# Performance work log

Hardware: AMD Instinct MI355X
Metric: run time of the kernel (lower is better)

Reference implementation:

```python
import jax, jax.numpy as jnp
import numpy as np

NB, NA, NC, NH, NW = 64, 5, 20, 38, 38
MAXT = 40
ANCHORS = jnp.array([[1.3221, 1.73145], [3.19275, 4.00944], [5.05587, 8.09892],
                     [9.47112, 4.84053], [11.2364, 10.0071]], dtype=jnp.float32)
OBJECT_SCALE, NOOBJECT_SCALE = 5.0, 1.0
CLASS_SCALE, COORD_SCALE = 1.0, 1.0
THRESH = 0.4


def setup_inputs() -> dict:
    key = jax.random.key(0)
    k1, k2, k3, k4 = jax.random.split(key, 4)
    output = jax.random.normal(k1, (NB, NA * (5 + NC), NH, NW), dtype=jnp.float32)
    cls_id = jax.random.randint(k2, (NB, MAXT), 0, NC).astype(jnp.float32)
    gxy = jax.random.uniform(k3, (NB, MAXT, 2), minval=0.05, maxval=0.95)
    gwh = jax.random.uniform(k4, (NB, MAXT, 2), minval=0.05, maxval=0.5)
    target = jnp.concatenate([cls_id[..., None], gxy, gwh], axis=-1).reshape(NB, MAXT * 5)
    return {"output": output, "target": target}


def iou_cwh(a, b):
    # boxes in (cx, cy, w, h)
    ax1, ax2 = a[..., 0] - a[..., 2] * 0.5, a[..., 0] + a[..., 2] * 0.5
    ay1, ay2 = a[..., 1] - a[..., 3] * 0.5, a[..., 1] + a[..., 3] * 0.5
    bx1, bx2 = b[..., 0] - b[..., 2] * 0.5, b[..., 0] + b[..., 2] * 0.5
    by1, by2 = b[..., 1] - b[..., 3] * 0.5, b[..., 1] + b[..., 3] * 0.5
    iw = jnp.maximum(jnp.minimum(ax2, bx2) - jnp.maximum(ax1, bx1), 0.0)
    ih = jnp.maximum(jnp.minimum(ay2, by2) - jnp.maximum(ay1, by1), 0.0)
    inter = iw * ih
    union = a[..., 2] * a[..., 3] + b[..., 2] * b[..., 3] - inter
    return inter / union


def smooth_l1_sum(p, t):
    d = jnp.abs(p - t)
    return jnp.sum(jnp.where(d < 1.0, 0.5 * d * d, d - 0.5))


def _forward(output, target):
    nB, nA, nC, nH, nW = NB, NA, NC, NH, NW
    out5 = output.reshape(nB, nA, 5 + nC, nH, nW)
    x = jax.nn.sigmoid(out5[:, :, 0])      # [nB,nA,nH,nW]
    y = jax.nn.sigmoid(out5[:, :, 1])
    w = out5[:, :, 2]
    h = out5[:, :, 3]
    conf = jax.nn.sigmoid(out5[:, :, 4])
    cls_logits = jnp.transpose(out5[:, :, 5:], (0, 1, 3, 4, 2))  # [nB,nA,nH,nW,nC]

    # --- decode predicted boxes (detached, mirrors use of .data in torch) ---
    sg = jax.lax.stop_gradient
    grid_x = jnp.arange(nW, dtype=jnp.float32)[None, None, None, :]
    grid_y = jnp.arange(nH, dtype=jnp.float32)[None, None, :, None]
    aw = ANCHORS[:, 0][None, :, None, None]
    ah = ANCHORS[:, 1][None, :, None, None]
    pred = jnp.stack([sg(x) + grid_x, sg(y) + grid_y,
                      jnp.exp(sg(w)) * aw, jnp.exp(sg(h)) * ah], axis=-1)  # [nB,nA,nH,nW,4]

    # --- build_targets (vectorized) ---
    tgt = target.reshape(nB, MAXT, 5)
    gcls = tgt[..., 0]
    gx, gy = tgt[..., 1] * nW, tgt[..., 2] * nH
    gw, gh = tgt[..., 3] * nW, tgt[..., 4] * nH
    # loop breaks at first zero gx: all later targets invalid
    valid = jnp.cumprod((tgt[..., 1] != 0).astype(jnp.float32), axis=1) > 0  # [nB,40]

    gt_boxes = jnp.stack([gx, gy, gw, gh], axis=-1)                 # [nB,40,4]
    pb = pred.reshape(nB, nA * nH * nW, 4)
    ious = iou_cwh(gt_boxes[:, :, None, :], pb[:, None, :, :])      # [nB,40,nAnchors]
    ious = jnp.where(valid[:, :, None], ious, 0.0)
    cur_ious = jnp.max(ious, axis=1)                                # [nB,nAnchors]
    conf_mask = jnp.where(cur_ious > THRESH, 0.0, NOOBJECT_SCALE).reshape(nB, nA, nH, nW)

    # best anchor per GT: IoU of zero-centered (w,h) boxes
    aws, ahs = ANCHORS[:, 0], ANCHORS[:, 1]
    inter = jnp.minimum(gw[..., None], aws) * jnp.minimum(gh[..., None], ahs)
    a_iou = inter / (gw[..., None] * gh[..., None] + aws * ahs - inter)  # [nB,40,nA]
    best_n = jnp.argmax(a_iou, axis=-1)                                  # [nB,40]

    gi = jnp.clip(gx.astype(jnp.int32), 0, nW - 1)
    gj = jnp.clip(gy.astype(jnp.int32), 0, nH - 1)
    bidx = jnp.broadcast_to(jnp.arange(nB)[:, None], (nB, MAXT))
    gi_s = jnp.where(valid, gi, nW)  # out-of-bounds -> dropped scatter
    idx = (bidx, best_n, gj, gi_s)

    pred_sel = pred[bidx, best_n, gj, gi]        # [nB,40,4]
    t_iou = iou_cwh(gt_boxes, pred_sel)          # [nB,40]
    aw_b, ah_b = aws[best_n], ahs[best_n]
    vtx = gx - gi.astype(jnp.float32)
    vty = gy - gj.astype(jnp.float32)
    vtw = jnp.log(gw / aw_b)
    vth = jnp.log(gh / ah_b)

    zeros = jnp.zeros((nB, nA, nH, nW), dtype=jnp.float32)
    coord_mask = zeros.at[idx].set(1.0, mode='drop')
    cls_mask = coord_mask  # identical writes in torch code
    conf_mask = conf_mask.at[idx].set(OBJECT_SCALE, mode='drop')
    tx = zeros.at[idx].set(vtx, mode='drop')
    ty = zeros.at[idx].set(vty, mode='drop')
    tw = zeros.at[idx].set(vtw, mode='drop')
    th = zeros.at[idx].set(vth, mode='drop')
    tconf = zeros.at[idx].set(t_iou, mode='drop')
    tcls = jnp.zeros((nB, nA, nH, nW), dtype=jnp.int32).at[idx].set(gcls.astype(jnp.int32), mode='drop')

    coord_mask = sg(coord_mask); cls_mask = sg(cls_mask)
    conf_mask = sg(conf_mask)
    tx, ty, tw, th, tconf = sg(tx), sg(ty), sg(tw), sg(th), sg(tconf)

    # --- losses ---
    loss_x = COORD_SCALE * smooth_l1_sum(x * coord_mask, tx * coord_mask) / 2.0
    loss_y = COORD_SCALE * smooth_l1_sum(y * coord_mask, ty * coord_mask) / 2.0
    loss_w = COORD_SCALE * smooth_l1_sum(w * coord_mask, tw * coord_mask) / 2.0
    loss_h = COORD_SCALE * smooth_l1_sum(h * coord_mask, th * coord_mask) / 2.0
    cm = jnp.sqrt(conf_mask)
    loss_conf = jnp.sum((conf * cm - tconf * cm) ** 2) / 2.0
    # focal loss (gamma=2, sum) over cls-masked locations
    logp = jax.nn.log_softmax(cls_logits, axis=-1)
    logpt = jnp.take_along_axis(logp, tcls[..., None], axis=-1)[..., 0]
    pt = jnp.exp(logpt)
    fl = -((1.0 - pt) ** 2) * logpt
    loss_cls = CLASS_SCALE * jnp.sum(cls_mask * fl)

    loss_box = loss_x + loss_y + loss_w + loss_h + loss_conf
    loss = loss_box + loss_cls
    return loss, loss_cls, loss_box


def reference(output, target):
    return _forward(output, target)
```

## Files before the change

### kernel.cpp

```cpp
#include <hip/hip_runtime.h>

#define NB 64
#define NA 5
#define NC 20
#define NH 38
#define NW 38
#define MAXT 40
#define CS (NH * NW)
#define CELLS_PER_B (NA * CS)
#define TPB 256
#define CPT 2
#define CHUNK_CELLS (TPB * CPT)
#define CHUNKS 16
#define NBLK (NB * CHUNKS)
#define IOUC (0.4f / 1.4f)

__constant__ float c_aw[NA] = {1.3221f, 3.19275f, 5.05587f, 9.47112f, 11.2364f};
__constant__ float c_ah[NA] = {1.73145f, 4.00944f, 8.09892f, 4.84053f, 10.0071f};

__device__ __forceinline__ float sl1(float d) {
    d = fabsf(d);
    return (d < 1.0f) ? 0.5f * d * d : d - 0.5f;
}
__device__ __forceinline__ float sigm(float x) {
    return __builtin_amdgcn_rcpf(1.0f + __expf(-x));
}

__global__ __launch_bounds__(TPB) void region_kernel(
    const float* __restrict__ outp, const float* __restrict__ tgt,
    float2* __restrict__ partials)
{
    __shared__ float4 s_box[MAXT];
    __shared__ alignas(16) float s_ga[MAXT];
    __shared__ int    s_key[MAXT];

    const int b     = blockIdx.x >> 4;
    const int chunk = blockIdx.x & 15;
    const int tid   = threadIdx.x;

    const int cbase = chunk * CHUNK_CELLS + tid;
    float xo[CPT], yo[CPT], wo[CPT], ho[CPT], co[CPT];
    bool live[CPT];
    #pragma unroll
    for (int u = 0; u < CPT; ++u) {
        const int c  = cbase + u * TPB;
        live[u] = (c < CELLS_PER_B);
        const int cc = live[u] ? c : (CELLS_PER_B - 1);
        const int a  = cc / CS, r = cc - a * CS;
        const float* cell = outp + (size_t)((b * NA + a) * (5 + NC)) * CS + r;
        xo[u] = cell[0];      yo[u] = cell[CS];
        wo[u] = cell[2 * CS]; ho[u] = cell[3 * CS];
        co[u] = cell[4 * CS];
    }

    float w_gx = 0.f, w_gy = 0.f, w_gw = 0.f, w_gh = 0.f;
    int   w_bn = 0, w_gi = 0, w_gj = 0, w_cls = 0, mykey = -1;
    bool  w_valid = false;

    if (tid < 64) {
        const bool is_t = tid < MAXT;
        const float* tb = tgt + b * (MAXT * 5) + tid * 5;
        float t0 = 0.f, t1 = 0.f, t2 = 0.f, t3 = 0.f, t4 = 0.f;
        if (is_t) { t0 = tb[0]; t1 = tb[1]; t2 = tb[2]; t3 = tb[3]; t4 = tb[4]; }
        const unsigned long long nz = __ballot(is_t && (t1 != 0.0f));
        const bool valid = is_t && ((~nz & (((1ull << tid) << 1) - 1ull)) == 0ull);
        if (is_t) {
            float4 mybox = make_float4(3e30f, 3e30f, -3e30f, -3e30f);
            float  myga  = 0.0f;
            if (valid) {
                const float gx = t1 * NW, gy = t2 * NH, gw = t3 * NW, gh = t4 * NH;
                int bn = 0; float best = -1.0f;
                #pragma unroll
                for (int a = 0; a < NA; ++a) {
                    const float inter = fminf(gw, c_aw[a]) * fminf(gh, c_ah[a]);
                    const float aiou  = inter / (gw * gh + c_aw[a] * c_ah[a] - inter);
                    if (aiou > best) { best = aiou; bn = a; }
                }
                const int gi = min(max((int)gx, 0), NW - 1);
                const int gj = min(max((int)gy, 0), NH - 1);
                mybox = make_float4(gx - 0.5f * gw, gy - 0.5f * gh,
                                    gx + 0.5f * gw, gy + 0.5f * gh);
                myga  = IOUC * (gw * gh);
                mykey = bn * CS + gj * NW + gi;
                w_gx = gx; w_gy = gy; w_gw = gw; w_gh = gh;
                w_bn = bn; w_gi = gi; w_gj = gj; w_cls = (int)t0; w_valid = true;
            }
            s_box[tid] = mybox; s_ga[tid] = myga; s_key[tid] = valid ? mykey : -1;
        }
    }

    float px1[CPT], px2[CPT], py1[CPT], py2[CPT], p04[CPT], scv[CPT];
    #pragma unroll
    for (int u = 0; u < CPT; ++u) {
        const int c = cbase + u * TPB;
        const int cc = live[u] ? c : 0;
        const int a = cc / CS, r = cc - a * CS;
        const int j = r / NW,  i = r - j * NW;
        const float sx = sigm(xo[u]), sy = sigm(yo[u]);
        scv[u] = live[u] ? sigm(co[u]) : 0.0f;
        const float pxc = sx + (float)i, pyc = sy + (float)j;
        const float pw = __expf(wo[u]) * c_aw[a], ph = __expf(ho[u]) * c_ah[a];
        px1[u] = pxc - 0.5f * pw; px2[u] = pxc + 0.5f * pw;
        py1[u] = pyc - 0.5f * ph; py2[u] = pyc + 0.5f * ph;
        p04[u] = IOUC * (pw * ph);
    }

    __syncthreads();

    float box_sum = 0.0f, cls_sum = 0.0f;

    if (chunk == CHUNKS - 1 && w_valid) {
        bool last = true;
        for (int tp = tid + 1; tp < MAXT; ++tp) last &= (s_key[tp] != mykey);
        if (last) {
            const float* cell = outp + (size_t)((b * NA + w_bn) * (5 + NC)) * CS
                                + (w_gj * NW + w_gi);
            const float xw = cell[0],      yw = cell[CS];
            const float ww = cell[2 * CS], hw = cell[3 * CS], cw = cell[4 * CS];
            float cls_v[NC];
            #pragma unroll
            for (int q = 0; q < NC; ++q) cls_v[q] = cell[(5 + q) * CS];

            const float sx = sigm(xw), sy = sigm(yw), sc = sigm(cw);
            const float pxc = sx + (float)w_gi, pyc = sy + (float)w_gj;
            const float pw = __expf(ww) * c_aw[w_bn], ph = __expf(hw) * c_ah[w_bn];
            const float wx1 = pxc - 0.5f * pw, wx2 = pxc + 0.5f * pw;
            const float wy1 = pyc - 0.5f * ph, wy2 = pyc + 0.5f * ph;
            const float pa = pw * ph, wp04 = IOUC * (pw * ph);

            bool flag = false;
            for (int t = 0; t < MAXT; ++t) {
                const float4 bx = s_box[t];
                const float iw = fminf(wx2, bx.z) - fmaxf(wx1, bx.x);
                const float ih = fminf(wy2, bx.w) - fmaxf(wy1, bx.y);
                const float inter = fmaxf(iw, 0.0f) * fmaxf(ih, 0.0f);
                flag = flag | (inter > wp04 + s_ga[t]);
            }
            const float cmd = flag ? 0.0f : 1.0f;

            const float gx1 = w_gx - 0.5f * w_gw, gx2 = w_gx + 0.5f * w_gw;
            const float gy1 = w_gy - 0.5f * w_gh, gy2 = w_gy + 0.5f * w_gh;
            const float iw = fminf(wx2, gx2) - fmaxf(wx1, gx1);
            const float ih = fminf(wy2, gy2) - fmaxf(wy1, gy1);
            const float inter = fmaxf(iw, 0.f) * fmaxf(ih, 0.f);
            const float tconf = inter / (w_gw * w_gh + pa - inter);

            const float dc = sc - tconf;
            box_sum += 2.5f * dc * dc - 0.5f * cmd * sc * sc;

            const float vtx = w_gx - (float)w_gi, vty = w_gy - (float)w_gj;
            const float vtw = __logf(w_gw / c_aw[w_bn]);
            const float vth = __logf(w_gh / c_ah[w_bn]);
            box_sum += 0.5f * (sl1(sx - vtx) + sl1(sy - vty) +
                               sl1(ww - vtw) + sl1(hw - vth));

            float m = -1e30f;
            #pragma unroll
            for (int q = 0; q < NC; ++q) m = fmaxf(m, cls_v[q]);
            float se = 0.f, lt = 0.f;
            #pragma unroll
            for (int q = 0; q < NC; ++q) {
                se += __expf(cls_v[q] - m);
                if (q == w_cls) lt = cls_v[q];
            }
            const float logpt = lt - (m + __logf(se));
            const float pt = __expf(logpt);
            const float om = 1.0f - pt;
            cls_sum += -(om * om) * logpt;
        }
    } else if (chunk != CHUNKS - 1) {
        bool flag[CPT];
        #pragma unroll
        for (int u = 0; u < CPT; ++u) flag[u] = false;

        #pragma unroll 2
        for (int t4 = 0; t4 < MAXT; t4 += 4) {
            const float4 ga4 = *reinterpret_cast<const float4*>(&s_ga[t4]);
            #pragma unroll
            for (int k = 0; k < 4; ++k) {
                const float4 bx = s_box[t4 + k];
                const float  ga = (k == 0) ? ga4.x : (k == 1) ? ga4.y
                                 : (k == 2) ? ga4.z : ga4.w;
                #pragma unroll
                for (int u = 0; u < CPT; ++u) {
                    const float iw = fminf(px2[u], bx.z) - fmaxf(px1[u], bx.x);
                    const float ih = fminf(py2[u], bx.w) - fmaxf(py1[u], bx.y);
                    const float inter = fmaxf(iw, 0.0f) * fmaxf(ih, 0.0f);
                    flag[u] = flag[u] | (inter > p04[u] + ga);
                }
            }
        }

        #pragma unroll
        for (int u = 0; u < CPT; ++u) {
            if (!flag[u]) box_sum += 0.5f * scv[u] * scv[u];
        }
    }

    #pragma unroll
    for (int off = 32; off > 0; off >>= 1) {
        box_sum += __shfl_down(box_sum, off);
        cls_sum += __shfl_down(cls_sum, off);
    }
    __shared__ float red[8];
    const int wv = tid >> 6, ln = tid & 63;
    if (ln == 0) { red[wv] = box_sum; red[4 + wv] = cls_sum; }
    __syncthreads();
    if (tid == 0) {
        partials[blockIdx.x] = make_float2(red[0] + red[1] + red[2] + red[3],
                                           red[4] + red[5] + red[6] + red[7]);
    }
}

__global__ __launch_bounds__(256) void finalize_kernel(
    const float2* __restrict__ partials, float* __restrict__ o)
{
    const int tid = threadIdx.x;
    float box = 0.0f, cls = 0.0f;
    #pragma unroll
    for (int k = 0; k < 4; ++k) {
        const float2 p = partials[tid + k * 256];
        box += p.x; cls += p.y;
    }
    #pragma unroll
    for (int off = 32; off > 0; off >>= 1) {
        box += __shfl_down(box, off);
        cls += __shfl_down(cls, off);
    }
    __shared__ float red[8];
    const int wv = tid >> 6, ln = tid & 63;
    if (ln == 0) { red[wv] = box; red[4 + wv] = cls; }
    __syncthreads();
    if (tid == 0) {
        const float boxT = red[0] + red[1] + red[2] + red[3];
        const float clsT = red[4] + red[5] + red[6] + red[7];
        o[0] = boxT + clsT;
        o[1] = clsT;
        o[2] = boxT;
    }
}

extern "C" void kernel_launch(void* const* d_in, const int* in_sizes, int n_in,
                              void* d_out, int out_size, void* d_ws, size_t ws_size,
                              hipStream_t stream)
{
    const float* outp = (const float*)d_in[0];
    const float* tgt  = (const float*)d_in[1];
    float2* partials  = (float2*)d_ws;

    region_kernel<<<dim3(NBLK), dim3(TPB), 0, stream>>>(outp, tgt, partials);
    finalize_kernel<<<1, 256, 0, stream>>>(partials, (float*)d_out);
}
```

Baseline: 18.05 us.

## Broadcast target boxes via readlane per wave, split last-chunk path from LDS

The non-last chunks now compute the target boxes redundantly in every wave and broadcast them with readlane, with no shared-memory staging. This removes the block-wide barrier and the LDS reads from the main IoU loop, which is now fully unrolled. The last chunk keeps the shared-memory path and its own barrier. In exchange, every wave repeats the target loads and box math, and the unrolled loop adds 200 readlane instructions.

```diff
diff --git a/kernel.cpp b/kernel.cpp
--- a/kernel.cpp
+++ b/kernel.cpp
@@ -25,169 +25,189 @@
 __device__ __forceinline__ float sigm(float x) {
     return __builtin_amdgcn_rcpf(1.0f + __expf(-x));
 }
+__device__ __forceinline__ float rdlane(float v, int l) {
+    return __int_as_float(__builtin_amdgcn_readlane(__float_as_int(v), l));
+}
 
 __global__ __launch_bounds__(TPB) void region_kernel(
     const float* __restrict__ outp, const float* __restrict__ tgt,
     float2* __restrict__ partials)
 {
     __shared__ float4 s_box[MAXT];
-    __shared__ alignas(16) float s_ga[MAXT];
+    __shared__ float  s_ga[MAXT];
     __shared__ int    s_key[MAXT];
+    __shared__ float  red[8];
 
     const int b     = blockIdx.x >> 4;
     const int chunk = blockIdx.x & 15;
     const int tid   = threadIdx.x;
-
-    const int cbase = chunk * CHUNK_CELLS + tid;
-    float xo[CPT], yo[CPT], wo[CPT], ho[CPT], co[CPT];
-    bool live[CPT];
-    #pragma unroll
-    for (int u = 0; u < CPT; ++u) {
-        const int c  = cbase + u * TPB;
-        live[u] = (c < CELLS_PER_B);
-        const int cc = live[u] ? c : (CELLS_PER_B - 1);
-        const int a  = cc / CS, r = cc - a * CS;
-        const float* cell = outp + (size_t)((b * NA + a) * (5 + NC)) * CS + r;
-        xo[u] = cell[0];      yo[u] = cell[CS];
-        wo[u] = cell[2 * CS]; ho[u] = cell[3 * CS];
-        co[u] = cell[4 * CS];
-    }
-
-    float w_gx = 0.f, w_gy = 0.f, w_gw = 0.f, w_gh = 0.f;
-    int   w_bn = 0, w_gi = 0, w_gj = 0, w_cls = 0, mykey = -1;
-    bool  w_valid = false;
-
-    if (tid < 64) {
-        const bool is_t = tid < MAXT;
-        const float* tb = tgt + b * (MAXT * 5) + tid * 5;
-        float t0 = 0.f, t1 = 0.f, t2 = 0.f, t3 = 0.f, t4 = 0.f;
-        if (is_t) { t0 = tb[0]; t1 = tb[1]; t2 = tb[2]; t3 = tb[3]; t4 = tb[4]; }
-        const unsigned long long nz = __ballot(is_t && (t1 != 0.0f));
-        const bool valid = is_t && ((~nz & (((1ull << tid) << 1) - 1ull)) == 0ull);
-        if (is_t) {
-            float4 mybox = make_float4(3e30f, 3e30f, -3e30f, -3e30f);
-            float  myga  = 0.0f;
+    const int lane  = tid & 63;
+
+    float box_sum = 0.0f, cls_sum = 0.0f;
+
+    if (chunk == CHUNKS - 1) {
+        float w_gx = 0.f, w_gy = 0.f, w_gw = 0.f, w_gh = 0.f;
+        int   w_bn = 0, w_gi = 0, w_gj = 0, w_cls = 0, mykey = -1;
+        bool  w_valid = false;
+
+        if (tid < 64) {
+            const bool is_t = tid < MAXT;
+            const float* tb = tgt + b * (MAXT * 5) + tid * 5;
+            float t0 = 0.f, t1 = 0.f, t2 = 0.f, t3 = 0.f, t4 = 0.f;
+            if (is_t) { t0 = tb[0]; t1 = tb[1]; t2 = tb[2]; t3 = tb[3]; t4 = tb[4]; }
+            const unsigned long long nz = __ballot(is_t && (t1 != 0.0f));
+            const bool valid = is_t && ((~nz & (((1ull << tid) << 1) - 1ull)) == 0ull);
+            if (is_t) {
+                float4 mybox = make_float4(3e30f, 3e30f, -3e30f, -3e30f);
+                float  myga  = 0.0f;
+                if (valid) {
+                    const float gx = t1 * NW, gy = t2 * NH, gw = t3 * NW, gh = t4 * NH;
+                    int bn = 0; float best = -1.0f;
+                    #pragma unroll
+                    for (int a = 0; a < NA; ++a) {
+                        const float inter = fminf(gw, c_aw[a]) * fminf(gh, c_ah[a]);
+                        const float aiou  = inter / (gw * gh + c_aw[a] * c_ah[a] - inter);
+                        if (aiou > best) { best = aiou; bn = a; }
+                    }
+                    const int gi = min(max((int)gx, 0), NW - 1);
+                    const int gj = min(max((int)gy, 0), NH - 1);
+                    mybox = make_float4(gx - 0.5f * gw, gy - 0.5f * gh,
+                                        gx + 0.5f * gw, gy + 0.5f * gh);
+                    myga  = IOUC * (gw * gh);
+                    mykey = bn * CS + gj * NW + gi;
+                    w_gx = gx; w_gy = gy; w_gw = gw; w_gh = gh;
+                    w_bn = bn; w_gi = gi; w_gj = gj; w_cls = (int)t0; w_valid = true;
+                }
+                s_box[tid] = mybox; s_ga[tid] = myga; s_key[tid] = valid ? mykey : -1;
+            }
+        }
+        __syncthreads();
+
+        if (w_valid) {
+            bool last = true;
+            for (int tp = tid + 1; tp < MAXT; ++tp) last &= (s_key[tp] != mykey);
+            if (last) {
+                const float* cell = outp + (size_t)((b * NA + w_bn) * (5 + NC)) * CS
+                                    + (w_gj * NW + w_gi);
+                const float xw = cell[0],      yw = cell[CS];
+                const float ww = cell[2 * CS], hw = cell[3 * CS], cw = cell[4 * CS];
+                float cls_v[NC];
+                #pragma unroll
+                for (int q = 0; q < NC; ++q) cls_v[q] = cell[(5 + q) * CS];
+
+                const float sx = sigm(xw), sy = sigm(yw), sc = sigm(cw);
+                const float pxc = sx + (float)w_gi, pyc = sy + (float)w_gj;
+                const float pw = __expf(ww) * c_aw[w_bn], ph = __expf(hw) * c_ah[w_bn];
+                const float wx1 = pxc - 0.5f * pw, wx2 = pxc + 0.5f * pw;
+                const float wy1 = pyc - 0.5f * ph, wy2 = pyc + 0.5f * ph;
+                const float pa = pw * ph, wp04 = IOUC * (pw * ph);
+
+                bool flag = false;
+                for (int t = 0; t < MAXT; ++t) {
+                    const float4 bx = s_box[t];
+                    const float iw = fminf(wx2, bx.z) - fmaxf(wx1, bx.x);
+                    const float ih = fminf(wy2, bx.w) - fmaxf(wy1, bx.y);
+                    const float inter = fmaxf(iw, 0.0f) * fmaxf(ih, 0.0f);
+                    flag = flag | (inter > wp04 + s_ga[t]);
+                }
+                const float cmd = flag ? 0.0f : 1.0f;
+
+                const float gx1 = w_gx - 0.5f * w_gw, gx2 = w_gx + 0.5f * w_gw;
+                const float gy1 = w_gy - 0.5f * w_gh, gy2 = w_gy + 0.5f * w_gh;
+                const float iw = fminf(wx2, gx2) - fmaxf(wx1, gx1);
+                const float ih = fminf(wy2, gy2) - fmaxf(wy1, gy1);
+                const float inter = fmaxf(iw, 0.f) * fmaxf(ih, 0.f);
+                const float tconf = inter / (w_gw * w_gh + pa - inter);
+
+                const float dc = sc - tconf;
+                box_sum += 2.5f * dc * dc - 0.5f * cmd * sc * sc;
+
+                const float vtx = w_gx - (float)w_gi, vty = w_gy - (float)w_gj;
+                const float vtw = __logf(w_gw / c_aw[w_bn]);
+                const float vth = __logf(w_gh / c_ah[w_bn]);
+                box_sum += 0.5f * (sl1(sx - vtx) + sl1(sy - vty) +
+                                   sl1(ww - vtw) + sl1(hw - vth));
+
+                float m = -1e30f;
+                #pragma unroll
+                for (int q = 0; q < NC; ++q) m = fmaxf(m, cls_v[q]);
+                float se = 0.f, lt = 0.f;
+                #pragma unroll
+                for (int q = 0; q < NC; ++q) {
+                    se += __expf(cls_v[q] - m);
+                    if (q == w_cls) lt = cls_v[q];
+                }
+                const float logpt = lt - (m + __logf(se));
+                const float pt = __expf(logpt);
+                const float om = 1.0f - pt;
+                cls_sum += -(om * om) * logpt;
+            }
+        }
+    } else {
+        const int cbase = chunk * CHUNK_CELLS + tid;
+        float xo[CPT], yo[CPT], wo[CPT], ho[CPT], co[CPT];
+        bool live[CPT];
+        #pragma unroll
+        for (int u = 0; u < CPT; ++u) {
+            const int c  = cbase + u * TPB;
+            live[u] = (c < CELLS_PER_B);
+            const int cc = live[u] ? c : (CELLS_PER_B - 1);
+            const int a  = cc / CS, r = cc - a * CS;
+            const float* cell = outp + (size_t)((b * NA + a) * (5 + NC)) * CS + r;
+            xo[u] = cell[0];      yo[u] = cell[CS];
+            wo[u] = cell[2 * CS]; ho[u] = cell[3 * CS];
+            co[u] = cell[4 * CS];
+        }
+
+        float x1v = 3e30f, y1v = 3e30f, x2v = -3e30f, y2v = -3e30f, gav = 0.0f;
+        {
+            const bool is_t = lane < MAXT;
+            const float* tb = tgt + b * (MAXT * 5) + lane * 5;
+            float t1 = 0.f, t2 = 0.f, t3 = 0.f, t4 = 0.f;
+            if (is_t) { t1 = tb[1]; t2 = tb[2]; t3 = tb[3]; t4 = tb[4]; }
+            const unsigned long long nz = __ballot(is_t && (t1 != 0.0f));
+            const bool valid = is_t && ((~nz & (((1ull << lane) << 1) - 1ull)) == 0ull);
             if (valid) {
                 const float gx = t1 * NW, gy = t2 * NH, gw = t3 * NW, gh = t4 * NH;
-                int bn = 0; float best = -1.0f;
-                #pragma unroll
-                for (int a = 0; a < NA; ++a) {
-                    const float inter = fminf(gw, c_aw[a]) * fminf(gh, c_ah[a]);
-                    const float aiou  = inter / (gw * gh + c_aw[a] * c_ah[a] - inter);
-                    if (aiou > best) { best = aiou; bn = a; }
-                }
-                const int gi = min(max((int)gx, 0), NW - 1);
-                const int gj = min(max((int)gy, 0), NH - 1);
-                mybox = make_float4(gx - 0.5f * gw, gy - 0.5f * gh,
-                                    gx + 0.5f * gw, gy + 0.5f * gh);
-                myga  = IOUC * (gw * gh);
-                mykey = bn * CS + gj * NW + gi;
-                w_gx = gx; w_gy = gy; w_gw = gw; w_gh = gh;
-                w_bn = bn; w_gi = gi; w_gj = gj; w_cls = (int)t0; w_valid = true;
-            }
-            s_box[tid] = mybox; s_ga[tid] = myga; s_key[tid] = valid ? mykey : -1;
-        }
-    }
-
-    float px1[CPT], px2[CPT], py1[CPT], py2[CPT], p04[CPT], scv[CPT];
-    #pragma unroll
-    for (int u = 0; u < CPT; ++u) {
-        const int c = cbase + u * TPB;
-        const int cc = live[u] ? c : 0;
-        const int a = cc / CS, r = cc - a * CS;
-        const int j = r / NW,  i = r - j * NW;
-        const float sx = sigm(xo[u]), sy = sigm(yo[u]);
-        scv[u] = live[u] ? sigm(co[u]) : 0.0f;
-        const float pxc = sx + (float)i, pyc = sy + (float)j;
-        const float pw = __expf(wo[u]) * c_aw[a], ph = __expf(ho[u]) * c_ah[a];
-        px1[u] = pxc - 0.5f * pw; px2[u] = pxc + 0.5f * pw;
-        py1[u] = pyc - 0.5f * ph; py2[u] = pyc + 0.5f * ph;
-        p04[u] = IOUC * (pw * ph);
-    }
-
-    __syncthreads();
-
-    float box_sum = 0.0f, cls_sum = 0.0f;
-
-    if (chunk == CHUNKS - 1 && w_valid) {
-        bool last = true;
-        for (int tp = tid + 1; tp < MAXT; ++tp) last &= (s_key[tp] != mykey);
-        if (last) {
-            const float* cell = outp + (size_t)((b * NA + w_bn) * (5 + NC)) * CS
-                                + (w_gj * NW + w_gi);
-            const float xw = cell[0],      yw = cell[CS];
-            const float ww = cell[2 * CS], hw = cell[3 * CS], cw = cell[4 * CS];
-            float cls_v[NC];
+                x1v = gx - 0.5f * gw; y1v = gy - 0.5f * gh;
+                x2v = gx + 0.5f * gw; y2v = gy + 0.5f * gh;
+                gav = IOUC * (gw * gh);
+            }
+        }
+
+        float px1[CPT], px2[CPT], py1[CPT], py2[CPT], p04[CPT], scv[CPT];
+        #pragma unroll
+        for (int u = 0; u < CPT; ++u) {
+            const int c = cbase + u * TPB;
+            const int cc = live[u] ? c : 0;
+            const int a = cc / CS, r = cc - a * CS;
+            const int j = r / NW,  i = r - j * NW;
+            const float sx = sigm(xo[u]), sy = sigm(yo[u]);
+            scv[u] = live[u] ? sigm(co[u]) : 0.0f;
+            const float pxc = sx + (float)i, pyc = sy + (float)j;
+            const float pw = __expf(wo[u]) * c_aw[a], ph = __expf(ho[u]) * c_ah[a];
+            px1[u] = pxc - 0.5f * pw; px2[u] = pxc + 0.5f * pw;
+            py1[u] = pyc - 0.5f * ph; py2[u] = pyc + 0.5f * ph;
+            p04[u] = IOUC * (pw * ph);
+        }
+
+        bool flag[CPT];
+        #pragma unroll
+        for (int u = 0; u < CPT; ++u) flag[u] = false;
+
+        #pragma unroll
+        for (int t = 0; t < MAXT; ++t) {
+            const float bx1 = rdlane(x1v, t);
+            const float by1 = rdlane(y1v, t);
+            const float bx2 = rdlane(x2v, t);
+            const float by2 = rdlane(y2v, t);
+            const float ga  = rdlane(gav, t);
             #pragma unroll
-            for (int q = 0; q < NC; ++q) cls_v[q] = cell[(5 + q) * CS];
-
-            const float sx = sigm(xw), sy = sigm(yw), sc = sigm(cw);
-            const float pxc = sx + (float)w_gi, pyc = sy + (float)w_gj;
-            const float pw = __expf(ww) * c_aw[w_bn], ph = __expf(hw) * c_ah[w_bn];
-            const float wx1 = pxc - 0.5f * pw, wx2 = pxc + 0.5f * pw;
-            const float wy1 = pyc - 0.5f * ph, wy2 = pyc + 0.5f * ph;
-            const float pa = pw * ph, wp04 = IOUC * (pw * ph);
-
-            bool flag = false;
-            for (int t = 0; t < MAXT; ++t) {
-                const float4 bx = s_box[t];
-                const float iw = fminf(wx2, bx.z) - fmaxf(wx1, bx.x);
-                const float ih = fminf(wy2, bx.w) - fmaxf(wy1, bx.y);
+            for (int u = 0; u < CPT; ++u) {
+                const float iw = fminf(px2[u], bx2) - fmaxf(px1[u], bx1);
+                const float ih = fminf(py2[u], by2) - fmaxf(py1[u], by1);
                 const float inter = fmaxf(iw, 0.0f) * fmaxf(ih, 0.0f);
-                flag = flag | (inter > wp04 + s_ga[t]);
-            }
-            const float cmd = flag ? 0.0f : 1.0f;
-
-            const float gx1 = w_gx - 0.5f * w_gw, gx2 = w_gx + 0.5f * w_gw;
-            const float gy1 = w_gy - 0.5f * w_gh, gy2 = w_gy + 0.5f * w_gh;
-            const float iw = fminf(wx2, gx2) - fmaxf(wx1, gx1);
-            const float ih = fminf(wy2, gy2) - fmaxf(wy1, gy1);
-            const float inter = fmaxf(iw, 0.f) * fmaxf(ih, 0.f);
-            const float tconf = inter / (w_gw * w_gh + pa - inter);
-
-            const float dc = sc - tconf;
-            box_sum += 2.5f * dc * dc - 0.5f * cmd * sc * sc;
-
-            const float vtx = w_gx - (float)w_gi, vty = w_gy - (float)w_gj;
-            const float vtw = __logf(w_gw / c_aw[w_bn]);
-            const float vth = __logf(w_gh / c_ah[w_bn]);
-            box_sum += 0.5f * (sl1(sx - vtx) + sl1(sy - vty) +
-                               sl1(ww - vtw) + sl1(hw - vth));
-
-            float m = -1e30f;
-            #pragma unroll
-            for (int q = 0; q < NC; ++q) m = fmaxf(m, cls_v[q]);
-            float se = 0.f, lt = 0.f;
-            #pragma unroll
-            for (int q = 0; q < NC; ++q) {
-                se += __expf(cls_v[q] - m);
-                if (q == w_cls) lt = cls_v[q];
-            }
-            const float logpt = lt - (m + __logf(se));
-            const float pt = __expf(logpt);
-            const float om = 1.0f - pt;
-            cls_sum += -(om * om) * logpt;
-        }
-    } else if (chunk != CHUNKS - 1) {
-        bool flag[CPT];
-        #pragma unroll
-        for (int u = 0; u < CPT; ++u) flag[u] = false;
-
-        #pragma unroll 2
-        for (int t4 = 0; t4 < MAXT; t4 += 4) {
-            const float4 ga4 = *reinterpret_cast<const float4*>(&s_ga[t4]);
-            #pragma unroll
-            for (int k = 0; k < 4; ++k) {
-                const float4 bx = s_box[t4 + k];
-                const float  ga = (k == 0) ? ga4.x : (k == 1) ? ga4.y
-                                 : (k == 2) ? ga4.z : ga4.w;
-                #pragma unroll
-                for (int u = 0; u < CPT; ++u) {
-                    const float iw = fminf(px2[u], bx.z) - fmaxf(px1[u], bx.x);
-                    const float ih = fminf(py2[u], bx.w) - fmaxf(py1[u], bx.y);
-                    const float inter = fmaxf(iw, 0.0f) * fmaxf(ih, 0.0f);
-                    flag[u] = flag[u] | (inter > p04[u] + ga);
-                }
+                flag[u] = flag[u] | (inter > p04[u] + ga);
             }
         }
 
@@ -202,7 +222,6 @@
         box_sum += __shfl_down(box_sum, off);
         cls_sum += __shfl_down(cls_sum, off);
     }
-    __shared__ float red[8];
     const int wv = tid >> 6, ln = tid & 63;
     if (ln == 0) { red[wv] = box_sum; red[4 + wv] = cls_sum; }
     __syncthreads();
```

New measurement: 18.43 us. +2.1%, slower.
